# Optimization experiments

Measured on AMD Instinct MI355X. Metric: run time of the kernel, lower is better.

The kernel has to match this reference:

```python
import jax, jax.numpy as jnp
import numpy as np

N = 50000    # nodes
E = 600000   # edges
F = 128      # num_features
ED = 16      # edge_dim
H = 4        # heads
D = 32       # per-head channels = hidden_units // heads
HID = H * D  # hidden_units = 128
C = 10       # num_classes


def _lin(k, fan_in, fan_out):
    # torch.nn.Linear-style init scale
    return jax.random.uniform(k, (fan_in, fan_out), jnp.float32, -1.0, 1.0) / np.sqrt(fan_in)


def setup_inputs() -> dict:
    key = jax.random.key(0)
    ks = jax.random.split(key, 24)
    inp = {
        "x": jax.random.normal(ks[0], (N, F), jnp.float32),
        "edge_index": jax.random.randint(ks[1], (2, E), 0, N, dtype=jnp.int32),
        "edge_attr": jax.random.normal(ks[2], (E, ED), jnp.float32),
    }
    j = 3
    for l, ind in enumerate([F, HID]):
        specs = {"q": (ind, HID, True), "k": (ind, HID, True), "v": (ind, HID, True),
                 "e": (ED, HID, False), "s": (ind, HID, True)}
        for nm, (i, o, bias) in specs.items():
            inp[f"W{nm}{l}"] = _lin(ks[j], i, o); j += 1
            if bias:
                inp[f"b{nm}{l}"] = jnp.zeros((o,), jnp.float32)
    inp["Wout"] = _lin(ks[j], HID, C)
    inp["bout"] = jnp.zeros((C,), jnp.float32)
    return inp


def _transformer_conv(x, src, dst, eattr, Wq, bq, Wk, bk, Wv, bv, We, Ws, bs):
    # PyG TransformerConv: concat=True, root_weight=True, beta=False, eval dropout.
    n = x.shape[0]
    q = (x @ Wq + bq).reshape(n, H, D)
    k = (x @ Wk + bk).reshape(n, H, D)
    v = (x @ Wv + bv).reshape(n, H, D)
    e = (eattr @ We).reshape(-1, H, D)           # edge embedding, added to key and value
    kj = k[src] + e                              # [E, H, D]
    vj = v[src] + e                              # [E, H, D]
    logits = jnp.einsum("ehd,ehd->eh", q[dst], kj) / np.sqrt(D)
    m = jax.ops.segment_max(logits, dst, num_segments=n)          # [N, H]
    ex = jnp.exp(logits - m[dst])
    denom = jax.ops.segment_sum(ex, dst, num_segments=n)          # [N, H]
    alpha = ex / (denom[dst] + 1e-16)                             # PyG softmax eps
    out = jax.ops.segment_sum(vj * alpha[..., None], dst, num_segments=n)
    return out.reshape(n, HID) + x @ Ws + bs                      # concat heads + skip


def reference(x, edge_index, edge_attr,
              Wq0, bq0, Wk0, bk0, Wv0, bv0, We0, Ws0, bs0,
              Wq1, bq1, Wk1, bk1, Wv1, bv1, We1, Ws1, bs1,
              Wout, bout):
    src, dst = edge_index[0], edge_index[1]
    h = jax.nn.relu(_transformer_conv(x, src, dst, edge_attr,
                                      Wq0, bq0, Wk0, bk0, Wv0, bv0, We0, Ws0, bs0))
    h = jax.nn.relu(_transformer_conv(h, src, dst, edge_attr,
                                      Wq1, bq1, Wk1, bk1, Wv1, bv1, We1, Ws1, bs1))
    logits = h @ Wout + bout
    return jax.nn.log_softmax(logits, axis=1)
```

## Files before the change

kernel.cpp:

```cpp
#include <hip/hip_runtime.h>

typedef unsigned short u16;
typedef __attribute__((ext_vector_type(4))) u16 u16x4;
typedef __attribute__((ext_vector_type(8))) u16 u16x8;
typedef __attribute__((ext_vector_type(8))) short short8;
typedef __attribute__((ext_vector_type(4))) float f32x4;
typedef __attribute__((ext_vector_type(4))) float f4;

#define NN 50000
#define NE 600000
#define HEADS 4
#define DH 32
#define HIDU 128
#define NC 10
#define NBLK 196

__device__ __forceinline__ float bf2f(u16 u) {
    union { unsigned int i; float f; } c; c.i = ((unsigned int)u) << 16; return c.f;
}
__device__ __forceinline__ u16 f2bf(float f) {
    union { float f; unsigned int i; } c; c.f = f;
    unsigned int x = c.i;
    return (u16)((x + 0x7fffu + ((x >> 16) & 1u)) >> 16);
}
__device__ __forceinline__ float qadd_xor1(float v) {
    int o = __builtin_amdgcn_update_dpp(0, __float_as_int(v), 0xB1, 0xF, 0xF, true);
    return v + __int_as_float(o);
}
__device__ __forceinline__ float qadd_xor2(float v) {
    int o = __builtin_amdgcn_update_dpp(0, __float_as_int(v), 0x4E, 0xF, 0xF, true);
    return v + __int_as_float(o);
}

__global__ void k_zero(int* p, int n) {
    int i = blockIdx.x * blockDim.x + threadIdx.x;
    if (i < n) p[i] = 0;
}

__global__ void k_hist(const int* __restrict__ dst, int* __restrict__ deg) {
    int i = blockIdx.x * blockDim.x + threadIdx.x;
    if (i < NE) atomicAdd(&deg[dst[i]], 1);
}

__global__ __launch_bounds__(256) void scan_a(const int* __restrict__ deg,
                                              int* __restrict__ bsum) {
    __shared__ int red[4];
    int i = blockIdx.x * 256 + threadIdx.x;
    int v = (i < NN) ? deg[i] : 0;
    #pragma unroll
    for (int off = 1; off < 64; off <<= 1) v += __shfl_xor(v, off);
    if ((threadIdx.x & 63) == 0) red[threadIdx.x >> 6] = v;
    __syncthreads();
    if (threadIdx.x == 0) bsum[blockIdx.x] = red[0] + red[1] + red[2] + red[3];
}

__global__ __launch_bounds__(256) void scan_b(const int* __restrict__ bsum,
                                              int* __restrict__ boff,
                                              int* __restrict__ row_ptr) {
    __shared__ int s[256];
    int t = threadIdx.x;
    int v = (t < NBLK) ? bsum[t] : 0;
    s[t] = v;
    __syncthreads();
    for (int off = 1; off < 256; off <<= 1) {
        int x = (t >= off) ? s[t - off] : 0;
        __syncthreads();
        s[t] += x;
        __syncthreads();
    }
    if (t < NBLK) boff[t] = s[t] - v;
    if (t == 0) row_ptr[NN] = NE;
}

__global__ __launch_bounds__(256) void scan_c(const int* __restrict__ deg,
                                              const int* __restrict__ boff,
                                              int* __restrict__ row_ptr,
                                              int* __restrict__ cursor) {
    __shared__ int s[256];
    int t = threadIdx.x;
    int i = blockIdx.x * 256 + t;
    int v = (i < NN) ? deg[i] : 0;
    s[t] = v;
    __syncthreads();
    for (int off = 1; off < 256; off <<= 1) {
        int x = (t >= off) ? s[t - off] : 0;
        __syncthreads();
        s[t] += x;
        __syncthreads();
    }
    if (i < NN) {
        int r = boff[blockIdx.x] + s[t] - v;
        row_ptr[i] = r;
        cursor[i] = r;
    }
}

__global__ void k_scatter(const int* __restrict__ ei, const float* __restrict__ eattr,
                          int* __restrict__ cursor,
                          int* __restrict__ csr_src, u16* __restrict__ ea16) {
    int i = blockIdx.x * blockDim.x + threadIdx.x;
    if (i < NE) {
        int s = ei[i];
        int d = ei[NE + i];
        int pos = atomicAdd(&cursor[d], 1);
        csr_src[pos] = s;
        const f4* ep = (const f4*)(eattr + (size_t)i * 16);
        f4 a = ep[0], b = ep[1], c = ep[2], dd = ep[3];
        u16x8 o0, o1;
        #pragma unroll
        for (int j = 0; j < 4; j++) {
            o0[j] = f2bf(a[j]); o0[4 + j] = f2bf(b[j]);
            o1[j] = f2bf(c[j]); o1[4 + j] = f2bf(dd[j]);
        }
        *(u16x8*)(ea16 + (size_t)pos * 16)     = o0;
        *(u16x8*)(ea16 + (size_t)pos * 16 + 8) = o1;
    }
}

__global__ void k_cvtw(const float* w0, const float* w1, const float* w2, const float* w3,
                       const float* w4, const float* w5, const float* w6, const float* w7,
                       u16* __restrict__ hi, u16* __restrict__ lo) {
    const float* w;
    switch (blockIdx.x) {
        case 0: w = w0; break; case 1: w = w1; break;
        case 2: w = w2; break; case 3: w = w3; break;
        case 4: w = w4; break; case 5: w = w5; break;
        case 6: w = w6; break; default: w = w7; break;
    }
    u16* oh = hi + blockIdx.x * 16384;
    u16* ol = lo + blockIdx.x * 16384;
    for (int i = 0; i < 64; i++) {
        int idx = threadIdx.x + i * 256;
        int k = idx >> 7, n = idx & 127;
        float v = w[idx];
        u16 h = f2bf(v);
        float r = v - bf2f(h);
        oh[n * 128 + k] = h;
        ol[n * 128 + k] = f2bf(r);
    }
}

__global__ __launch_bounds__(256) void gemm_qkv(
    const float* __restrict__ X, const u16* __restrict__ WtHi,
    const float* __restrict__ b0, const float* __restrict__ b1,
    const float* __restrict__ b2,
    float* __restrict__ outq, u16* __restrict__ outk, u16* __restrict__ outv,
    int nrows)
{
    __shared__ u16 Bs[128 * 128];
    const int mat = blockIdx.y;
    const u16* wh = WtHi + mat * 16384;

    #pragma unroll
    for (int i = 0; i < 8; i++) {
        int idx = threadIdx.x + i * 256;
        int n = idx >> 4, g = idx & 15;
        *(u16x8*)(&Bs[n * 128 + ((g ^ (n & 15)) << 3)]) = *(const u16x8*)(wh + n * 128 + g * 8);
    }
    __syncthreads();

    const int wave = threadIdx.x >> 6, lane = threadIdx.x & 63;
    const int n0 = lane & 15;
    const int qw = lane >> 4;
    const int kq = qw * 8;

    const float* xp[2];
    #pragma unroll
    for (int rt = 0; rt < 2; rt++) {
        int arow = blockIdx.x * 128 + wave * 32 + rt * 16 + n0;
        int arow_c = arow < nrows ? arow : nrows - 1;
        xp[rt] = X + (size_t)arow_c * HIDU + kq;
    }

    f32x4 acc[2][8];
    #pragma unroll
    for (int rt = 0; rt < 2; rt++)
        #pragma unroll
        for (int nt = 0; nt < 8; nt++) acc[rt][nt] = (f32x4){0.f, 0.f, 0.f, 0.f};

    #pragma unroll
    for (int ks = 0; ks < 4; ks++) {
        short8 ah[2];
        #pragma unroll
        for (int rt = 0; rt < 2; rt++) {
            f4 a0 = *(const f4*)(xp[rt] + ks * 32);
            f4 a1 = *(const f4*)(xp[rt] + ks * 32 + 4);
            #pragma unroll
            for (int j = 0; j < 4; j++) {
                ah[rt][j]     = (short)(__float_as_uint(a0[j]) >> 16);
                ah[rt][4 + j] = (short)(__float_as_uint(a1[j]) >> 16);
            }
        }
        #pragma unroll
        for (int nt = 0; nt < 8; nt++) {
            const int boff = (nt * 16 + n0) * 128 + (((ks << 2) + qw) ^ n0) * 8;
            short8 bh = *(const short8*)(&Bs[boff]);
            #pragma unroll
            for (int rt = 0; rt < 2; rt++)
                acc[rt][nt] = __builtin_amdgcn_mfma_f32_16x16x32_bf16(ah[rt], bh, acc[rt][nt], 0, 0, 0);
        }
    }

    const float* bia = (mat == 0) ? b0 : (mat == 1) ? b1 : b2;
    #pragma unroll
    for (int rt = 0; rt < 2; rt++) {
        const int rbase = blockIdx.x * 128 + wave * 32 + rt * 16 + qw * 4;
        #pragma unroll
        for (int nt = 0; nt < 8; nt++) {
            int col = nt * 16 + n0;
            float bv = bia[col];
            #pragma unroll
            for (int r = 0; r < 4; r++) {
                int grow = rbase + r;
                if (grow < nrows) {
                    float v = acc[rt][nt][r] + bv;
                    if (mat == 0)      outq[(size_t)grow * HIDU + col] = v;
                    else if (mat == 1) outk[(size_t)grow * HIDU + col] = f2bf(v);
                    else               outv[(size_t)grow * HIDU + col] = f2bf(v);
                }
            }
        }
    }
}

__global__ __launch_bounds__(256) void gemm_s(
    const float* __restrict__ X,
    const u16* __restrict__ wh, const u16* __restrict__ wl,
    const float* __restrict__ bia, float* __restrict__ outs, int nrows)
{
    __shared__ u16 Bs[2 * 128 * 128];

    #pragma unroll
    for (int i = 0; i < 8; i++) {
        int idx = threadIdx.x + i * 256;
        int n = idx >> 4, g = idx & 15;
        int dst = n * 128 + ((g ^ (n & 15)) << 3);
        *(u16x8*)(&Bs[dst])         = *(const u16x8*)(wh + n * 128 + g * 8);
        *(u16x8*)(&Bs[16384 + dst]) = *(const u16x8*)(wl + n * 128 + g * 8);
    }
    __syncthreads();

    const int wave = threadIdx.x >> 6, lane = threadIdx.x & 63;
    const int n0 = lane & 15;
    const int qw = lane >> 4;
    const int kq = qw * 8;

    const float* xp[2];
    #pragma unroll
    for (int rt = 0; rt < 2; rt++) {
        int arow = blockIdx.x * 128 + wave * 32 + rt * 16 + n0;
        int arow_c = arow < nrows ? arow : nrows - 1;
        xp[rt] = X + (size_t)arow_c * HIDU + kq;
    }

    f32x4 acc[2][8];
    #pragma unroll
    for (int rt = 0; rt < 2; rt++)
        #pragma unroll
        for (int nt = 0; nt < 8; nt++) acc[rt][nt] = (f32x4){0.f, 0.f, 0.f, 0.f};

    #pragma unroll
    for (int ks = 0; ks < 4; ks++) {
        short8 ah[2], al[2];
        #pragma unroll
        for (int rt = 0; rt < 2; rt++) {
            f4 a0 = *(const f4*)(xp[rt] + ks * 32);
            f4 a1 = *(const f4*)(xp[rt] + ks * 32 + 4);
            #pragma unroll
            for (int j = 0; j < 4; j++) {
                unsigned u0 = __float_as_uint(a0[j]);
                unsigned u1 = __float_as_uint(a1[j]);
                ah[rt][j]     = (short)(u0 >> 16);
                ah[rt][4 + j] = (short)(u1 >> 16);
                float r0 = a0[j] - __uint_as_float(u0 & 0xffff0000u);
                float r1 = a1[j] - __uint_as_float(u1 & 0xffff0000u);
                al[rt][j]     = (short)(__float_as_uint(r0) >> 16);
                al[rt][4 + j] = (short)(__float_as_uint(r1) >> 16);
            }
        }
        #pragma unroll
        for (int nt = 0; nt < 8; nt++) {
            const int boff = (nt * 16 + n0) * 128 + (((ks << 2) + qw) ^ n0) * 8;
            short8 bh = *(const short8*)(&Bs[boff]);
            short8 bl = *(const short8*)(&Bs[16384 + boff]);
            #pragma unroll
            for (int rt = 0; rt < 2; rt++) {
                acc[rt][nt] = __builtin_amdgcn_mfma_f32_16x16x32_bf16(ah[rt], bh, acc[rt][nt], 0, 0, 0);
                acc[rt][nt] = __builtin_amdgcn_mfma_f32_16x16x32_bf16(al[rt], bh, acc[rt][nt], 0, 0, 0);
                acc[rt][nt] = __builtin_amdgcn_mfma_f32_16x16x32_bf16(ah[rt], bl, acc[rt][nt], 0, 0, 0);
            }
        }
    }

    #pragma unroll
    for (int rt = 0; rt < 2; rt++) {
        const int rbase = blockIdx.x * 128 + wave * 32 + rt * 16 + qw * 4;
        #pragma unroll
        for (int nt = 0; nt < 8; nt++) {
            int col = nt * 16 + n0;
            float bv = bia[col];
            #pragma unroll
            for (int r = 0; r < 4; r++) {
                int grow = rbase + r;
                if (grow < nrows) outs[(size_t)grow * HIDU + col] = acc[rt][nt][r] + bv;
            }
        }
    }
}

__global__ __launch_bounds__(256) void attn(
    const float* __restrict__ qb, const u16* __restrict__ kb, const u16* __restrict__ vb,
    const float* __restrict__ sb, const u16* __restrict__ ea16, const float* __restrict__ We,
    const int* __restrict__ row_ptr, const int* __restrict__ csr_src,
    float* __restrict__ hout_f32,
    const float* __restrict__ Wout, const float* __restrict__ bout,
    float* __restrict__ out_logits, int mode)
{
    __shared__ float WeS[4 * 513];
    __shared__ float WoS[HIDU * NC];
    __shared__ float boS[NC];
    __shared__ float hrowS[16 * 132];
    __shared__ float lgS[16 * 16];

    #pragma unroll
    for (int i = 0; i < 8; i++) {
        int idx = threadIdx.x + i * 256;
        int tt = idx >> 7, c = idx & 127;
        int h = c >> 5, j = c & 31;
        WeS[h * 513 + tt * 32 + j] = We[idx];
    }
    if (mode == 1) {
        for (int i = 0; i < 5; i++) {
            int idx = threadIdx.x + i * 256;
            if (idx < HIDU * NC) WoS[idx] = Wout[idx];
        }
        if (threadIdx.x < NC) boS[threadIdx.x] = bout[threadIdx.x];
    }
    __syncthreads();

    int gtid = blockIdx.x * 256 + threadIdx.x;
    int n   = gtid >> 4;
    int l16 = gtid & 15;
    int h   = l16 >> 2;
    int sub = l16 & 3;
    const int lane = threadIdx.x & 63;
    const float* WeH = &WeS[h * 513];
    const int j0  = sub * 8;
    const int ch0 = h * DH + j0;
    const int t0  = sub * 4;

    float qreg[8];
    float g4[4];
    {
        const f4* qp = (const f4*)(qb + (size_t)n * HIDU + h * DH);
        float q32[32];
        #pragma unroll
        for (int c = 0; c < 8; c++) {
            f4 x = qp[c];
            #pragma unroll
            for (int j = 0; j < 4; j++) q32[c * 4 + j] = x[j];
        }
        #pragma unroll
        for (int tt = 0; tt < 4; tt++) {
            float a = 0.f;
            #pragma unroll
            for (int j = 0; j < 32; j++) a += q32[j] * WeH[(t0 + tt) * 32 + j];
            g4[tt] = a;
        }
        #pragma unroll
        for (int j = 0; j < 8; j++) qreg[j] = q32[j0 + j];
    }

    float m = -INFINITY, l = 0.f;
    float O[8];
    float a4[4];
    #pragma unroll
    for (int j = 0; j < 8; j++) O[j] = 0.f;
    #pragma unroll
    for (int tt = 0; tt < 4; tt++) a4[tt] = 0.f;

    const int r0 = row_ptr[n], r1 = row_ptr[n + 1];
    const float inv = 0.17677669529663687f;

    for (int e = r0; e < r1; e += 2) {
        bool has2 = (e + 1 < r1);
        int e1i = has2 ? e + 1 : e;
        int s0 = csr_src[e];
        int s1 = csr_src[e1i];
        u16x4 e0 = *(const u16x4*)(ea16 + (size_t)e * 16 + t0);
        u16x4 e1 = *(const u16x4*)(ea16 + (size_t)e1i * 16 + t0);

        u16x8 k0 = *(const u16x8*)(kb + (size_t)s0 * HIDU + ch0);
        u16x8 v0 = *(const u16x8*)(vb + (size_t)s0 * HIDU + ch0);
        u16x8 k1 = *(const u16x8*)(kb + (size_t)s1 * HIDU + ch0);
        u16x8 v1 = *(const u16x8*)(vb + (size_t)s1 * HIDU + ch0);

        float ea0[4], ea1[4];
        #pragma unroll
        for (int tt = 0; tt < 4; tt++) { ea0[tt] = bf2f(e0[tt]); ea1[tt] = bf2f(e1[tt]); }

        float d0 = 0.f, d1 = 0.f;
        #pragma unroll
        for (int j = 0; j < 8; j++) {
            d0 += qreg[j] * bf2f(k0[j]);
            d1 += qreg[j] * bf2f(k1[j]);
        }
        #pragma unroll
        for (int tt = 0; tt < 4; tt++) {
            d0 += g4[tt] * ea0[tt];
            d1 += g4[tt] * ea1[tt];
        }
        d0 = qadd_xor1(d0);  d1 = qadd_xor1(d1);
        d0 = qadd_xor2(d0);  d1 = qadd_xor2(d1);

        float logit0 = d0 * inv;
        float logit1 = has2 ? d1 * inv : -INFINITY;
        float mn = fmaxf(m, fmaxf(logit0, logit1));
        float corr = __expf(m - mn);
        float w0 = __expf(logit0 - mn);
        float w1 = __expf(logit1 - mn);
        l = l * corr + w0 + w1;
        #pragma unroll
        for (int j = 0; j < 8; j++)
            O[j] = O[j] * corr + w0 * bf2f(v0[j]) + w1 * bf2f(v1[j]);
        #pragma unroll
        for (int tt = 0; tt < 4; tt++)
            a4[tt] = a4[tt] * corr + w0 * ea0[tt] + w1 * ea1[tt];
        m = mn;
    }

    float af[16];
    #pragma unroll
    for (int t = 0; t < 16; t++)
        af[t] = __shfl(a4[t & 3], (lane & ~3) | (t >> 2));

    float invl = 1.0f / (l + 1e-16f);
    const float* sp = sb + (size_t)n * HIDU + ch0;

    float vals[8];
    #pragma unroll
    for (int j = 0; j < 8; j++) {
        float ev = 0.f;
        #pragma unroll
        for (int t = 0; t < 16; t++) ev += af[t] * WeH[t * 32 + j0 + j];
        vals[j] = fmaxf((O[j] + ev) * invl + sp[j], 0.f);
    }

    if (mode == 0) {
        const size_t obase = (size_t)n * HIDU + ch0;
        f4 r0v, r1v;
        #pragma unroll
        for (int j = 0; j < 4; j++) { r0v[j] = vals[j]; r1v[j] = vals[4 + j]; }
        *(f4*)(hout_f32 + obase) = r0v;
        *(f4*)(hout_f32 + obase + 4) = r1v;
    } else {
        const int cb = threadIdx.x >> 4;
        float* hr = &hrowS[cb * 132];
        f4 w0v, w1v;
        #pragma unroll
        for (int j = 0; j < 4; j++) { w0v[j] = vals[j]; w1v[j] = vals[4 + j]; }
        *(f4*)(hr + ch0) = w0v;
        *(f4*)(hr + ch0 + 4) = w1v;
        if (l16 < NC) {
            float lg = boS[l16];
            for (int ch = 0; ch < HIDU; ch += 4) {
                f4 hv = *(const f4*)(hr + ch);
                #pragma unroll
                for (int j = 0; j < 4; j++) lg += hv[j] * WoS[(ch + j) * NC + l16];
            }
            lgS[cb * 16 + l16] = lg;
        }
        if (l16 < NC) {
            float lgc = lgS[cb * 16 + l16];
            float mx = -INFINITY;
            #pragma unroll
            for (int c = 0; c < NC; c++) mx = fmaxf(mx, lgS[cb * 16 + c]);
            float sum = 0.f;
            #pragma unroll
            for (int c = 0; c < NC; c++) sum += __expf(lgS[cb * 16 + c] - mx);
            float lse = mx + __logf(sum);
            out_logits[(size_t)n * NC + l16] = lgc - lse;
        }
    }
}

extern "C" void kernel_launch(void* const* d_in, const int* in_sizes, int n_in,
                              void* d_out, int out_size, void* d_ws, size_t ws_size,
                              hipStream_t stream) {
    const float* x     = (const float*)d_in[0];
    const int*   ei    = (const int*)d_in[1];
    const float* eattr = (const float*)d_in[2];
    const float *Wq0 = (const float*)d_in[3],  *bq0 = (const float*)d_in[4];
    const float *Wk0 = (const float*)d_in[5],  *bk0 = (const float*)d_in[6];
    const float *Wv0 = (const float*)d_in[7],  *bv0 = (const float*)d_in[8];
    const float *We0 = (const float*)d_in[9];
    const float *Ws0 = (const float*)d_in[10], *bs0 = (const float*)d_in[11];
    const float *Wq1 = (const float*)d_in[12], *bq1 = (const float*)d_in[13];
    const float *Wk1 = (const float*)d_in[14], *bk1 = (const float*)d_in[15];
    const float *Wv1 = (const float*)d_in[16], *bv1 = (const float*)d_in[17];
    const float *We1 = (const float*)d_in[18];
    const float *Ws1 = (const float*)d_in[19], *bs1 = (const float*)d_in[20];
    const float *Wout = (const float*)d_in[21], *bout = (const float*)d_in[22];

    char* p = (char*)d_ws;
    auto alloc = [&](size_t bytes) -> void* {
        void* r = (void*)p;
        p += (bytes + 255) & ~(size_t)255;
        return r;
    };
    int* deg      = (int*)alloc(NN * 4);
    int* row_ptr  = (int*)alloc((NN + 1) * 4);
    int* cursor   = (int*)alloc(NN * 4);
    int* bsum     = (int*)alloc(NBLK * 4);
    int* boff     = (int*)alloc(NBLK * 4);
    int* csr_src  = (int*)alloc((size_t)NE * 4);
    float* qb     = (float*)alloc((size_t)NN * HIDU * 4);
    u16* kb       = (u16*)alloc((size_t)NN * HIDU * 2);
    u16* vb       = (u16*)alloc((size_t)NN * HIDU * 2);
    float* sbuf   = (float*)alloc((size_t)NN * HIDU * 4);
    float* hbuf   = (float*)alloc((size_t)NN * HIDU * 4);
    u16* ea16     = (u16*)alloc((size_t)NE * 16 * 2);
    u16* wthi     = (u16*)alloc(8 * 16384 * 2);
    u16* wtlo     = (u16*)alloc(8 * 16384 * 2);

    k_zero<<<(NN + 255) / 256, 256, 0, stream>>>(deg, NN);
    k_hist<<<(NE + 255) / 256, 256, 0, stream>>>(ei + NE, deg);
    scan_a<<<NBLK, 256, 0, stream>>>(deg, bsum);
    scan_b<<<1, 256, 0, stream>>>(bsum, boff, row_ptr);
    scan_c<<<NBLK, 256, 0, stream>>>(deg, boff, row_ptr, cursor);
    k_scatter<<<(NE + 255) / 256, 256, 0, stream>>>(ei, eattr, cursor, csr_src, ea16);

    k_cvtw<<<8, 256, 0, stream>>>(Wq0, Wk0, Wv0, Ws0, Wq1, Wk1, Wv1, Ws1, wthi, wtlo);

    const int gm = (NN + 127) / 128;
    const int ga = (NN * 16) / 256;

    gemm_qkv<<<dim3(gm, 3), 256, 0, stream>>>(x, wthi, bq0, bk0, bv0, qb, kb, vb, NN);
    gemm_s<<<gm, 256, 0, stream>>>(x, wthi + 3 * 16384, wtlo + 3 * 16384, bs0, sbuf, NN);
    attn<<<ga, 256, 0, stream>>>(qb, kb, vb, sbuf, ea16, We0, row_ptr, csr_src,
                                 hbuf, Wout, bout, (float*)d_out, 0);
    gemm_qkv<<<dim3(gm, 3), 256, 0, stream>>>(hbuf, wthi + 4 * 16384, bq1, bk1, bv1, qb, kb, vb, NN);
    gemm_s<<<gm, 256, 0, stream>>>(hbuf, wthi + 7 * 16384, wtlo + 7 * 16384, bs1, sbuf, NN);
    attn<<<ga, 256, 0, stream>>>(qb, kb, vb, sbuf, ea16, We1, row_ptr, csr_src,
                                 hbuf, Wout, bout, (float*)d_out, 1);
}
```

Baseline: 469.2 us.

## Fold skip GEMM into single-pass bf16 QKV GEMM and vectorize attention inner loop

The separate three-pass split-bf16 skip-projection GEMM is dropped. The skip matrix becomes a fourth grid slice of the single-pass bf16 QKV GEMM, which removes one launch and two thirds of its MFMA work. The low-part weight conversion goes away with it. The attention kernel unpacks bf16 pairs through 32-bit words into float4 vectors and re-pads the edge-weight shared array, aiming to cut per-edge ALU work and LDS bank conflicts. The cost is lower precision on the skip path, since the error-compensation terms are gone.

```diff
diff --git a/kernel.cpp b/kernel.cpp
--- a/kernel.cpp
+++ b/kernel.cpp
@@ -1,8 +1,10 @@
 #include <hip/hip_runtime.h>
 
 typedef unsigned short u16;
+typedef unsigned int u32;
 typedef __attribute__((ext_vector_type(4))) u16 u16x4;
 typedef __attribute__((ext_vector_type(8))) u16 u16x8;
+typedef __attribute__((ext_vector_type(4))) u32 u32x4;
 typedef __attribute__((ext_vector_type(8))) short short8;
 typedef __attribute__((ext_vector_type(4))) float f32x4;
 typedef __attribute__((ext_vector_type(4))) float f4;
@@ -14,6 +16,8 @@
 #define HIDU 128
 #define NC 10
 #define NBLK 196
+#define WES_T 34
+#define WES_H 546
 
 __device__ __forceinline__ float bf2f(u16 u) {
     union { unsigned int i; float f; } c; c.i = ((unsigned int)u) << 16; return c.f;
@@ -23,6 +27,8 @@
     unsigned int x = c.i;
     return (u16)((x + 0x7fffu + ((x >> 16) & 1u)) >> 16);
 }
+__device__ __forceinline__ float lo_bf(u32 d) { return __uint_as_float(d << 16); }
+__device__ __forceinline__ float hi_bf(u32 d) { return __uint_as_float(d & 0xffff0000u); }
 __device__ __forceinline__ float qadd_xor1(float v) {
     int o = __builtin_amdgcn_update_dpp(0, __float_as_int(v), 0xB1, 0xF, 0xF, true);
     return v + __int_as_float(o);
@@ -119,7 +125,7 @@
 
 __global__ void k_cvtw(const float* w0, const float* w1, const float* w2, const float* w3,
                        const float* w4, const float* w5, const float* w6, const float* w7,
-                       u16* __restrict__ hi, u16* __restrict__ lo) {
+                       u16* __restrict__ hi) {
     const float* w;
     switch (blockIdx.x) {
         case 0: w = w0; break; case 1: w = w1; break;
@@ -128,24 +134,19 @@
         case 6: w = w6; break; default: w = w7; break;
     }
     u16* oh = hi + blockIdx.x * 16384;
-    u16* ol = lo + blockIdx.x * 16384;
     for (int i = 0; i < 64; i++) {
         int idx = threadIdx.x + i * 256;
         int k = idx >> 7, n = idx & 127;
-        float v = w[idx];
-        u16 h = f2bf(v);
-        float r = v - bf2f(h);
-        oh[n * 128 + k] = h;
-        ol[n * 128 + k] = f2bf(r);
-    }
-}
-
-__global__ __launch_bounds__(256) void gemm_qkv(
+        oh[n * 128 + k] = f2bf(w[idx]);
+    }
+}
+
+__global__ __launch_bounds__(256) void gemm_qkvs(
     const float* __restrict__ X, const u16* __restrict__ WtHi,
     const float* __restrict__ b0, const float* __restrict__ b1,
-    const float* __restrict__ b2,
+    const float* __restrict__ b2, const float* __restrict__ b3,
     float* __restrict__ outq, u16* __restrict__ outk, u16* __restrict__ outv,
-    int nrows)
+    float* __restrict__ outs, int nrows)
 {
     __shared__ u16 Bs[128 * 128];
     const int mat = blockIdx.y;
@@ -201,7 +202,7 @@
         }
     }
 
-    const float* bia = (mat == 0) ? b0 : (mat == 1) ? b1 : b2;
+    const float* bia = (mat == 0) ? b0 : (mat == 1) ? b1 : (mat == 2) ? b2 : b3;
     #pragma unroll
     for (int rt = 0; rt < 2; rt++) {
         const int rbase = blockIdx.x * 128 + wave * 32 + rt * 16 + qw * 4;
@@ -216,93 +217,9 @@
                     float v = acc[rt][nt][r] + bv;
                     if (mat == 0)      outq[(size_t)grow * HIDU + col] = v;
                     else if (mat == 1) outk[(size_t)grow * HIDU + col] = f2bf(v);
-                    else               outv[(size_t)grow * HIDU + col] = f2bf(v);
+                    else if (mat == 2) outv[(size_t)grow * HIDU + col] = f2bf(v);
+                    else               outs[(size_t)grow * HIDU + col] = v;
                 }
-            }
-        }
-    }
-}
-
-__global__ __launch_bounds__(256) void gemm_s(
-    const float* __restrict__ X,
-    const u16* __restrict__ wh, const u16* __restrict__ wl,
-    const float* __restrict__ bia, float* __restrict__ outs, int nrows)
-{
-    __shared__ u16 Bs[2 * 128 * 128];
-
-    #pragma unroll
-    for (int i = 0; i < 8; i++) {
-        int idx = threadIdx.x + i * 256;
-        int n = idx >> 4, g = idx & 15;
-        int dst = n * 128 + ((g ^ (n & 15)) << 3);
-        *(u16x8*)(&Bs[dst])         = *(const u16x8*)(wh + n * 128 + g * 8);
-        *(u16x8*)(&Bs[16384 + dst]) = *(const u16x8*)(wl + n * 128 + g * 8);
-    }
-    __syncthreads();
-
-    const int wave = threadIdx.x >> 6, lane = threadIdx.x & 63;
-    const int n0 = lane & 15;
-    const int qw = lane >> 4;
-    const int kq = qw * 8;
-
-    const float* xp[2];
-    #pragma unroll
-    for (int rt = 0; rt < 2; rt++) {
-        int arow = blockIdx.x * 128 + wave * 32 + rt * 16 + n0;
-        int arow_c = arow < nrows ? arow : nrows - 1;
-        xp[rt] = X + (size_t)arow_c * HIDU + kq;
-    }
-
-    f32x4 acc[2][8];
-    #pragma unroll
-    for (int rt = 0; rt < 2; rt++)
-        #pragma unroll
-        for (int nt = 0; nt < 8; nt++) acc[rt][nt] = (f32x4){0.f, 0.f, 0.f, 0.f};
-
-    #pragma unroll
-    for (int ks = 0; ks < 4; ks++) {
-        short8 ah[2], al[2];
-        #pragma unroll
-        for (int rt = 0; rt < 2; rt++) {
-            f4 a0 = *(const f4*)(xp[rt] + ks * 32);
-            f4 a1 = *(const f4*)(xp[rt] + ks * 32 + 4);
-            #pragma unroll
-            for (int j = 0; j < 4; j++) {
-                unsigned u0 = __float_as_uint(a0[j]);
-                unsigned u1 = __float_as_uint(a1[j]);
-                ah[rt][j]     = (short)(u0 >> 16);
-                ah[rt][4 + j] = (short)(u1 >> 16);
-                float r0 = a0[j] - __uint_as_float(u0 & 0xffff0000u);
-                float r1 = a1[j] - __uint_as_float(u1 & 0xffff0000u);
-                al[rt][j]     = (short)(__float_as_uint(r0) >> 16);
-                al[rt][4 + j] = (short)(__float_as_uint(r1) >> 16);
-            }
-        }
-        #pragma unroll
-        for (int nt = 0; nt < 8; nt++) {
-            const int boff = (nt * 16 + n0) * 128 + (((ks << 2) + qw) ^ n0) * 8;
-            short8 bh = *(const short8*)(&Bs[boff]);
-            short8 bl = *(const short8*)(&Bs[16384 + boff]);
-            #pragma unroll
-            for (int rt = 0; rt < 2; rt++) {
-                acc[rt][nt] = __builtin_amdgcn_mfma_f32_16x16x32_bf16(ah[rt], bh, acc[rt][nt], 0, 0, 0);
-                acc[rt][nt] = __builtin_amdgcn_mfma_f32_16x16x32_bf16(al[rt], bh, acc[rt][nt], 0, 0, 0);
-                acc[rt][nt] = __builtin_amdgcn_mfma_f32_16x16x32_bf16(ah[rt], bl, acc[rt][nt], 0, 0, 0);
-            }
-        }
-    }
-
-    #pragma unroll
-    for (int rt = 0; rt < 2; rt++) {
-        const int rbase = blockIdx.x * 128 + wave * 32 + rt * 16 + qw * 4;
-        #pragma unroll
-        for (int nt = 0; nt < 8; nt++) {
-            int col = nt * 16 + n0;
-            float bv = bia[col];
-            #pragma unroll
-            for (int r = 0; r < 4; r++) {
-                int grow = rbase + r;
-                if (grow < nrows) outs[(size_t)grow * HIDU + col] = acc[rt][nt][r] + bv;
             }
         }
     }
@@ -316,7 +233,7 @@
     const float* __restrict__ Wout, const float* __restrict__ bout,
     float* __restrict__ out_logits, int mode)
 {
-    __shared__ float WeS[4 * 513];
+    __shared__ float WeS[4 * WES_H];
     __shared__ float WoS[HIDU * NC];
     __shared__ float boS[NC];
     __shared__ float hrowS[16 * 132];
@@ -327,7 +244,7 @@
         int idx = threadIdx.x + i * 256;
         int tt = idx >> 7, c = idx & 127;
         int h = c >> 5, j = c & 31;
-        WeS[h * 513 + tt * 32 + j] = We[idx];
+        WeS[h * WES_H + tt * WES_T + j] = We[idx];
     }
     if (mode == 1) {
         for (int i = 0; i < 5; i++) {
@@ -344,12 +261,12 @@
     int h   = l16 >> 2;
     int sub = l16 & 3;
     const int lane = threadIdx.x & 63;
-    const float* WeH = &WeS[h * 513];
+    const float* WeH = &WeS[h * WES_H];
     const int j0  = sub * 8;
     const int ch0 = h * DH + j0;
     const int t0  = sub * 4;
 
-    float qreg[8];
+    f4 qa, qbv;
     float g4[4];
     {
         const f4* qp = (const f4*)(qb + (size_t)n * HIDU + h * DH);
@@ -364,20 +281,16 @@
         for (int tt = 0; tt < 4; tt++) {
             float a = 0.f;
             #pragma unroll
-            for (int j = 0; j < 32; j++) a += q32[j] * WeH[(t0 + tt) * 32 + j];
+            for (int j = 0; j < 32; j++) a += q32[j] * WeH[(t0 + tt) * WES_T + j];
             g4[tt] = a;
         }
         #pragma unroll
-        for (int j = 0; j < 8; j++) qreg[j] = q32[j0 + j];
+        for (int j = 0; j < 4; j++) { qa[j] = q32[j0 + j]; qbv[j] = q32[j0 + 4 + j]; }
     }
 
     float m = -INFINITY, l = 0.f;
-    float O[8];
-    float a4[4];
-    #pragma unroll
-    for (int j = 0; j < 8; j++) O[j] = 0.f;
-    #pragma unroll
-    for (int tt = 0; tt < 4; tt++) a4[tt] = 0.f;
+    f4 O0 = {0.f, 0.f, 0.f, 0.f}, O1 = {0.f, 0.f, 0.f, 0.f};
+    f4 a4 = {0.f, 0.f, 0.f, 0.f};
 
     const int r0 = row_ptr[n], r1 = row_ptr[n + 1];
     const float inv = 0.17677669529663687f;
@@ -390,26 +303,23 @@
         u16x4 e0 = *(const u16x4*)(ea16 + (size_t)e * 16 + t0);
         u16x4 e1 = *(const u16x4*)(ea16 + (size_t)e1i * 16 + t0);
 
-        u16x8 k0 = *(const u16x8*)(kb + (size_t)s0 * HIDU + ch0);
-        u16x8 v0 = *(const u16x8*)(vb + (size_t)s0 * HIDU + ch0);
-        u16x8 k1 = *(const u16x8*)(kb + (size_t)s1 * HIDU + ch0);
-        u16x8 v1 = *(const u16x8*)(vb + (size_t)s1 * HIDU + ch0);
-
-        float ea0[4], ea1[4];
-        #pragma unroll
-        for (int tt = 0; tt < 4; tt++) { ea0[tt] = bf2f(e0[tt]); ea1[tt] = bf2f(e1[tt]); }
-
-        float d0 = 0.f, d1 = 0.f;
-        #pragma unroll
-        for (int j = 0; j < 8; j++) {
-            d0 += qreg[j] * bf2f(k0[j]);
-            d1 += qreg[j] * bf2f(k1[j]);
-        }
-        #pragma unroll
-        for (int tt = 0; tt < 4; tt++) {
-            d0 += g4[tt] * ea0[tt];
-            d1 += g4[tt] * ea1[tt];
-        }
+        u32x4 k0 = *(const u32x4*)(kb + (size_t)s0 * HIDU + ch0);
+        u32x4 v0 = *(const u32x4*)(vb + (size_t)s0 * HIDU + ch0);
+        u32x4 k1 = *(const u32x4*)(kb + (size_t)s1 * HIDU + ch0);
+        u32x4 v1 = *(const u32x4*)(vb + (size_t)s1 * HIDU + ch0);
+
+        f4 k0a = {lo_bf(k0[0]), hi_bf(k0[0]), lo_bf(k0[1]), hi_bf(k0[1])};
+        f4 k0b = {lo_bf(k0[2]), hi_bf(k0[2]), lo_bf(k0[3]), hi_bf(k0[3])};
+        f4 k1a = {lo_bf(k1[0]), hi_bf(k1[0]), lo_bf(k1[1]), hi_bf(k1[1])};
+        f4 k1b = {lo_bf(k1[2]), hi_bf(k1[2]), lo_bf(k1[3]), hi_bf(k1[3])};
+        f4 ea0 = {bf2f(e0[0]), bf2f(e0[1]), bf2f(e0[2]), bf2f(e0[3])};
+        f4 ea1 = {bf2f(e1[0]), bf2f(e1[1]), bf2f(e1[2]), bf2f(e1[3])};
+        f4 g4v = {g4[0], g4[1], g4[2], g4[3]};
+
+        f4 acc0 = qa * k0a + qbv * k0b + g4v * ea0;
+        f4 acc1 = qa * k1a + qbv * k1b + g4v * ea1;
+        float d0 = acc0[0] + acc0[1] + acc0[2] + acc0[3];
+        float d1 = acc1[0] + acc1[1] + acc1[2] + acc1[3];
         d0 = qadd_xor1(d0);  d1 = qadd_xor1(d1);
         d0 = qadd_xor2(d0);  d1 = qadd_xor2(d1);
 
@@ -420,12 +330,14 @@
         float w0 = __expf(logit0 - mn);
         float w1 = __expf(logit1 - mn);
         l = l * corr + w0 + w1;
-        #pragma unroll
-        for (int j = 0; j < 8; j++)
-            O[j] = O[j] * corr + w0 * bf2f(v0[j]) + w1 * bf2f(v1[j]);
-        #pragma unroll
-        for (int tt = 0; tt < 4; tt++)
-            a4[tt] = a4[tt] * corr + w0 * ea0[tt] + w1 * ea1[tt];
+
+        f4 v0a = {lo_bf(v0[0]), hi_bf(v0[0]), lo_bf(v0[1]), hi_bf(v0[1])};
+        f4 v0b = {lo_bf(v0[2]), hi_bf(v0[2]), lo_bf(v0[3]), hi_bf(v0[3])};
+        f4 v1a = {lo_bf(v1[0]), hi_bf(v1[0]), lo_bf(v1[1]), hi_bf(v1[1])};
+        f4 v1b = {lo_bf(v1[2]), hi_bf(v1[2]), lo_bf(v1[3]), hi_bf(v1[3])};
+        O0 = O0 * corr + v0a * w0 + v1a * w1;
+        O1 = O1 * corr + v0b * w0 + v1b * w1;
+        a4 = a4 * corr + ea0 * w0 + ea1 * w1;
         m = mn;
     }
 
@@ -442,8 +354,9 @@
     for (int j = 0; j < 8; j++) {
         float ev = 0.f;
         #pragma unroll
-        for (int t = 0; t < 16; t++) ev += af[t] * WeH[t * 32 + j0 + j];
-        vals[j] = fmaxf((O[j] + ev) * invl + sp[j], 0.f);
+        for (int t = 0; t < 16; t++) ev += af[t] * WeH[t * WES_T + j0 + j];
+        float Oj = (j < 4) ? O0[j] : O1[j - 4];
+        vals[j] = fmaxf((Oj + ev) * invl + sp[j], 0.f);
     }
 
     if (mode == 0) {
@@ -521,7 +434,6 @@
     float* hbuf   = (float*)alloc((size_t)NN * HIDU * 4);
     u16* ea16     = (u16*)alloc((size_t)NE * 16 * 2);
     u16* wthi     = (u16*)alloc(8 * 16384 * 2);
-    u16* wtlo     = (u16*)alloc(8 * 16384 * 2);
 
     k_zero<<<(NN + 255) / 256, 256, 0, stream>>>(deg, NN);
     k_hist<<<(NE + 255) / 256, 256, 0, stream>>>(ei + NE, deg);
@@ -530,17 +442,17 @@
     scan_c<<<NBLK, 256, 0, stream>>>(deg, boff, row_ptr, cursor);
     k_scatter<<<(NE + 255) / 256, 256, 0, stream>>>(ei, eattr, cursor, csr_src, ea16);
 
-    k_cvtw<<<8, 256, 0, stream>>>(Wq0, Wk0, Wv0, Ws0, Wq1, Wk1, Wv1, Ws1, wthi, wtlo);
+    k_cvtw<<<8, 256, 0, stream>>>(Wq0, Wk0, Wv0, Ws0, Wq1, Wk1, Wv1, Ws1, wthi);
 
     const int gm = (NN + 127) / 128;
     const int ga = (NN * 16) / 256;
 
-    gemm_qkv<<<dim3(gm, 3), 256, 0, stream>>>(x, wthi, bq0, bk0, bv0, qb, kb, vb, NN);
-    gemm_s<<<gm, 256, 0, stream>>>(x, wthi + 3 * 16384, wtlo + 3 * 16384, bs0, sbuf, NN);
+    gemm_qkvs<<<dim3(gm, 4), 256, 0, stream>>>(x, wthi, bq0, bk0, bv0, bs0,
+                                               qb, kb, vb, sbuf, NN);
     attn<<<ga, 256, 0, stream>>>(qb, kb, vb, sbuf, ea16, We0, row_ptr, csr_src,
                                  hbuf, Wout, bout, (float*)d_out, 0);
-    gemm_qkv<<<dim3(gm, 3), 256, 0, stream>>>(hbuf, wthi + 4 * 16384, bq1, bk1, bv1, qb, kb, vb, NN);
-    gemm_s<<<gm, 256, 0, stream>>>(hbuf, wthi + 7 * 16384, wtlo + 7 * 16384, bs1, sbuf, NN);
+    gemm_qkvs<<<dim3(gm, 4), 256, 0, stream>>>(hbuf, wthi + 4 * 16384, bq1, bk1, bv1, bs1,
+                                               qb, kb, vb, sbuf, NN);
     attn<<<ga, 256, 0, stream>>>(qb, kb, vb, sbuf, ea16, We1, row_ptr, csr_src,
                                  hbuf, Wout, bout, (float*)d_out, 1);
 }
```

New measurement: 457.9 us. -2.4%, faster.
